# Performance work log

Hardware: AMD Instinct MI355X
Metric: run time of the kernel (lower is better)

Reference implementation:

```python
import jax, jax.numpy as jnp
import numpy as np

B, T, P, U = 2, 50, 5111, 64


def setup_inputs() -> dict:
    key = jax.random.key(0)
    ks = jax.random.split(key, 12)
    data_target = jax.random.randint(ks[0], (B, T), 0, P)
    data_cor = jax.random.randint(ks[1], (B, T), 0, 2)
    # X: bi-LSTM max-pooled problem encodings [P, 2U]
    X = jax.random.normal(ks[2], (P, 2 * U), dtype=jnp.float32) * 0.1
    # cos_X: cosine similarity of X with itself (as in call_encode)
    norm = jnp.sqrt(jnp.sum(X * X, axis=1))
    cos_X = (X @ X.T) / (norm[:, None] * norm[None, :])
    # causal lower-triangular aggregation mask [T, T]
    trimatrix = jnp.tril(jnp.ones((T, T), dtype=jnp.float32))
    # frozen embedding2 table [2, 4U]
    emb2 = jax.random.uniform(ks[3], (2, 4 * U), minval=-1.0, maxval=1.0, dtype=jnp.float32)
    # LSTM params (keras gate order i,f,c,o), input dim 4U
    s = 0.1549193338
    Wk = jax.random.uniform(ks[4], (4 * U, 4 * U), minval=-s, maxval=s, dtype=jnp.float32)
    Wr = jax.random.normal(ks[5], (U, 4 * U), dtype=jnp.float32) * 0.05  # orthogonal-ish stand-in
    bl = jnp.concatenate([jnp.zeros((U,)), jnp.ones((U,)), jnp.zeros((2 * U,))]).astype(jnp.float32)  # unit forget bias
    s1 = 0.1732050808
    W1 = jax.random.uniform(ks[6], (3 * U, 50), minval=-s1, maxval=s1, dtype=jnp.float32)
    b1 = jnp.zeros((50,), dtype=jnp.float32)
    s2 = 0.3429971703
    W2 = jax.random.uniform(ks[7], (50, 1), minval=-s2, maxval=s2, dtype=jnp.float32)
    b2 = jnp.zeros((1,), dtype=jnp.float32)
    return {"data_target": data_target, "data_cor": data_cor, "num_pro": P,
            "X": X, "cos_X": cos_X, "trimatrix": trimatrix, "emb2": emb2,
            "Wk": Wk, "Wr": Wr, "bl": bl, "W1": W1, "b1": b1, "W2": W2, "b2": b2}


def _lstm(x, Wk, Wr, bl):
    # x: [B, T, D] -> h: [B, T, U]; keras LSTM math, gate order i,f,g,o
    u = Wr.shape[0]
    xT = jnp.swapaxes(x, 0, 1)  # [T, B, D]
    h0 = jnp.zeros((x.shape[0], u), x.dtype)
    c0 = jnp.zeros((x.shape[0], u), x.dtype)

    def step(carry, xt):
        h, c = carry
        z = xt @ Wk + h @ Wr + bl
        i, f, g, o = jnp.split(z, 4, axis=-1)
        c = jax.nn.sigmoid(f) * c + jax.nn.sigmoid(i) * jnp.tanh(g)
        h = jax.nn.sigmoid(o) * jnp.tanh(c)
        return (h, c), h

    _, hs = jax.lax.scan(step, (h0, c0), xT)
    return jnp.swapaxes(hs, 0, 1)


def reference(data_target, data_cor, num_pro, X, cos_X, trimatrix, emb2, Wk, Wr, bl, W1, b1, W2, b2):
    # one_hot @ X == gather
    t_X = X[data_target]                             # [B,T,2U]
    t_X = jnp.concatenate([t_X, t_X], axis=-1)       # [B,T,4U]
    xt = t_X * emb2[data_cor]                        # [B,T,4U]
    ht = _lstm(xt, Wk, Wr, bl)                       # [B,T,U]
    # attention aggregation: a[b,t,p] = cos_X[target[b,t], p]
    a = cos_X[data_target]                           # [B,T,P]
    # ajhj[b,s,p,u] = sum_t trimatrix[t,s] * a[b,t,p] * ht[b,t,u]
    ajhj = jnp.einsum('btp,btu,ts->bspu', a, ht, trimatrix)  # [B,T,P,U]
    XX = jnp.broadcast_to(X[None, None], (ajhj.shape[0], ajhj.shape[1], num_pro, X.shape[1]))
    hatt = jnp.concatenate([ajhj, XX], axis=-1)      # [B,T,P,3U]
    r = jax.nn.relu(hatt @ W1 + b1)                  # [B,T,P,50]
    r = r @ W2 + b2                                  # [B,T,P,1]
    return r
```

## Files before the change

### kernel.cpp

```cpp
#include <hip/hip_runtime.h>
#include <math.h>

#define B_ 2
#define T_ 50
#define P_ 5111
#define U_ 64

typedef float v2f __attribute__((ext_vector_type(2)));

#define QPERM(x, ctrl)                                                        \
  __int_as_float(__builtin_amdgcn_mov_dpp(__float_as_int(x), (ctrl), 0xf, 0xf, true))

__global__ __launch_bounds__(256) void zx_kernel(
    const int* __restrict__ tgt, const int* __restrict__ cor,
    const float* __restrict__ X, const float* __restrict__ emb2,
    const float* __restrict__ Wk, float* __restrict__ ZX) {
  const int bt = blockIdx.x;
  const int k  = threadIdx.x;
  __shared__ float xe[256];
  const int t_ = tgt[bt], c_ = cor[bt];
  xe[k] = X[t_ * 128 + (k & 127)] * emb2[c_ * 256 + k];
  __syncthreads();
  float z = 0.f;
#pragma unroll 8
  for (int d = 0; d < 256; ++d)
    z = fmaf(xe[d], Wk[d * 256 + k], z);
  ZX[bt * 256 + k] = z;
}

__global__ __launch_bounds__(256) void lstm_xwt_kernel(
    const float* __restrict__ ZX, const float* __restrict__ Wr,
    const float* __restrict__ bl, const float* __restrict__ W1,
    const float* __restrict__ X, const float* __restrict__ b1,
    float* __restrict__ G, float* __restrict__ XWT) {
  const int blk = blockIdx.x;
  const int k   = threadIdx.x;

  if (blk >= B_) {
    __shared__ float xrow[4][128];
    const int sub = k >> 6, lane = k & 63;
    const int p = (blk - B_) * 4 + sub;
    if (p < P_) {
      xrow[sub][lane]      = X[p * 128 + lane];
      xrow[sub][64 + lane] = X[p * 128 + 64 + lane];
    }
    __syncthreads();
    if (p < P_ && lane < 50) {
      float acc = b1[lane];
#pragma unroll 16
      for (int u = 0; u < 128; ++u)
        acc = fmaf(xrow[sub][u], W1[(64 + u) * 50 + lane], acc);
      XWT[lane * P_ + p] = acc;
    }
    return;
  }

  const int b   = blk;
  const int g   = k & 3;
  const int u   = k >> 2;
  const int col = g * 64 + u;
  __shared__ __align__(16) float H_s[T_ + 1][64];
  __shared__ __align__(16) float W1_s[64 * 50];

  v2f w2[32];
#pragma unroll
  for (int i = 0; i < 32; ++i) {
    v2f t; t.x = Wr[(2 * i) * 256 + col]; t.y = Wr[(2 * i + 1) * 256 + col];
    w2[i] = t;
  }
  const float blv = bl[col];
  float znext = ZX[(b * T_) * 256 + col];
  for (int i = k; i < 64 * 50; i += 256) W1_s[i] = W1[i];
  if (k < 64) H_s[0][k] = 0.f;
  float c = 0.f;
  __syncthreads();

  for (int t = 0; t < T_; ++t) {
    const float zcur = znext;
    if (t + 1 < T_) znext = ZX[(b * T_ + t + 1) * 256 + col];
    const float4* h4 = (const float4*)&H_s[t][0];
    v2f a0 = {0.f, 0.f}, a1 = {0.f, 0.f}, a2 = {0.f, 0.f}, a3 = {0.f, 0.f};
#pragma unroll
    for (int q = 0; q < 16; ++q) {
      const float4 hq = h4[q];
      v2f hlo; hlo.x = hq.x; hlo.y = hq.y;
      v2f hhi; hhi.x = hq.z; hhi.y = hq.w;
      if (q & 1) {
        a2 = __builtin_elementwise_fma(hlo, w2[2 * q], a2);
        a3 = __builtin_elementwise_fma(hhi, w2[2 * q + 1], a3);
      } else {
        a0 = __builtin_elementwise_fma(hlo, w2[2 * q], a0);
        a1 = __builtin_elementwise_fma(hhi, w2[2 * q + 1], a1);
      }
    }
    const v2f as = (a0 + a2) + (a1 + a3);
    const float z = as.x + as.y + zcur + blv;
    const bool isg2 = (g == 2);
    const float arg = isg2 ? (2.f * z) : (-z);
    const float e   = __expf(arg);
    const float v   = __fdividef(1.f, 1.f + e);
    const float res = isg2 ? fmaf(-2.f, v, 1.f) : v;
    const float v1 = QPERM(res, 177);
    const float v2 = QPERM(res, 78);
    const float v3 = QPERM(res, 27);
    const float ig = (g == 0) ? res : (g == 1) ? v1 : (g == 2) ? v2 : v3;
    const float fg = (g == 1) ? res : (g == 0) ? v1 : (g == 3) ? v2 : v3;
    const float gg = (g == 2) ? res : (g == 3) ? v1 : (g == 0) ? v2 : v3;
    const float og = (g == 3) ? res : (g == 2) ? v1 : (g == 1) ? v2 : v3;
    c = fmaf(fg, c, ig * gg);
    const float th = fmaf(-2.f, __fdividef(1.f, 1.f + __expf(2.f * c)), 1.f);
    if (g == 0) H_s[t + 1][u] = og * th;
    __syncthreads();
  }

  const v2f* W1_2 = (const v2f*)W1_s;
  v2f*       G_2  = (v2f*)G;
  for (int task = k; task < T_ * 25; task += 256) {
    const int t  = task / 25;
    const int jp = task % 25;
    const float* hrow = &H_s[t + 1][0];
    v2f acc = {0.f, 0.f};
#pragma unroll
    for (int u2 = 0; u2 < 64; ++u2) {
      v2f hb; hb.x = hrow[u2]; hb.y = hrow[u2];
      acc = __builtin_elementwise_fma(hb, W1_2[u2 * 25 + jp], acc);
    }
    G_2[b * (T_ * 25) + task] = acc;
  }
}

__global__ __launch_bounds__(256) void out_kernel(
    const int* __restrict__ tgt, const float* __restrict__ cosX,
    const float* __restrict__ G, const float* __restrict__ XWT,
    const float* __restrict__ W2, const float* __restrict__ b2,
    float* __restrict__ out) {
  const int b   = blockIdx.y;
  const int tid = threadIdx.x;
  const int p   = blockIdx.x * 256 + tid;
  __shared__ __align__(16) float G_s[T_ * 50];
  __shared__ __align__(16) float W2_s[50];
  __shared__ int tgt_s[T_];
  for (int i = tid; i < T_ * 50; i += 256) G_s[i] = G[b * T_ * 50 + i];
  if (tid < 50) {
    W2_s[tid]  = W2[tid];
    tgt_s[tid] = tgt[b * T_ + tid];
  }
  __syncthreads();
  if (p >= P_) return;

  float av[T_];
#pragma unroll
  for (int s = 0; s < T_; ++s) av[s] = cosX[tgt_s[s] * P_ + p];

  v2f S2[25];
#pragma unroll
  for (int jj = 0; jj < 25; ++jj) {
    v2f t; t.x = XWT[(2 * jj) * P_ + p]; t.y = XWT[(2 * jj + 1) * P_ + p];
    S2[jj] = t;
  }
  const v2f* W2_2 = (const v2f*)W2_s;
  const float b2v = b2[0];
  const v2f zero2 = {0.f, 0.f};
#pragma unroll
  for (int s = T_ - 1; s >= 0; --s) {
    const v2f* G2 = (const v2f*)&G_s[s * 50];
    v2f av2; av2.x = av[s]; av2.y = av[s];
    v2f acc2; acc2.x = b2v; acc2.y = 0.f;
#pragma unroll
    for (int jj = 0; jj < 25; ++jj) {
      S2[jj] = __builtin_elementwise_fma(av2, G2[jj], S2[jj]);
      const v2f r = __builtin_elementwise_max(S2[jj], zero2);
      acc2 = __builtin_elementwise_fma(r, W2_2[jj], acc2);
    }
    out[(b * T_ + s) * P_ + p] = acc2.x + acc2.y;
  }
}

extern "C" void kernel_launch(void* const* d_in, const int* in_sizes, int n_in,
                              void* d_out, int out_size, void* d_ws, size_t ws_size,
                              hipStream_t stream) {
  const int*   tgt  = (const int*)d_in[0];
  const int*   cor  = (const int*)d_in[1];
  const float* X    = (const float*)d_in[3];
  const float* cosX = (const float*)d_in[4];
  const float* emb2 = (const float*)d_in[6];
  const float* Wk   = (const float*)d_in[7];
  const float* Wr   = (const float*)d_in[8];
  const float* bl   = (const float*)d_in[9];
  const float* W1   = (const float*)d_in[10];
  const float* b1   = (const float*)d_in[11];
  const float* W2   = (const float*)d_in[12];
  const float* b2   = (const float*)d_in[13];
  float* out = (float*)d_out;

  float* ws  = (float*)d_ws;
  float* ZX  = ws;
  float* G   = ws + 25600;
  float* XWT = ws + 30600;

  const int xw_blocks = (P_ + 3) / 4;
  zx_kernel<<<dim3(B_ * T_), dim3(256), 0, stream>>>(tgt, cor, X, emb2, Wk, ZX);
  lstm_xwt_kernel<<<dim3(B_ + xw_blocks), dim3(256), 0, stream>>>(
      ZX, Wr, bl, W1, X, b1, G, XWT);
  out_kernel<<<dim3((P_ + 255) / 256, B_), dim3(256), 0, stream>>>(
      tgt, cosX, G, XWT, W2, b2, out);
}
```

Before: 248.4 us.

## Split output kernel over time chunks and move XWT into the pre-kernel

The output kernel gets a third grid dimension of 5 chunks over the time axis. Each block redundantly accumulates the suffix of later timesteps without the ReLU/W2 part, then emits outputs only for its own 10 timesteps. The goal is more blocks (the old grid was only 40 blocks) and shorter serial chains, at the cost of redundant FMA work and repeated cosX reads. The X@W1 precompute also moves out of the LSTM launch into the ZX kernel, so the LSTM kernel runs alone with 2 blocks.

```diff
diff --git a/kernel.cpp b/kernel.cpp
--- a/kernel.cpp
+++ b/kernel.cpp
@@ -5,57 +5,60 @@
 #define T_ 50
 #define P_ 5111
 #define U_ 64
+#define SC_ 10
+#define CH_ 5
 
 typedef float v2f __attribute__((ext_vector_type(2)));
 
 #define QPERM(x, ctrl)                                                        \
   __int_as_float(__builtin_amdgcn_mov_dpp(__float_as_int(x), (ctrl), 0xf, 0xf, true))
 
-__global__ __launch_bounds__(256) void zx_kernel(
+__global__ __launch_bounds__(256) void pre_kernel(
     const int* __restrict__ tgt, const int* __restrict__ cor,
     const float* __restrict__ X, const float* __restrict__ emb2,
-    const float* __restrict__ Wk, float* __restrict__ ZX) {
-  const int bt = blockIdx.x;
-  const int k  = threadIdx.x;
-  __shared__ float xe[256];
-  const int t_ = tgt[bt], c_ = cor[bt];
-  xe[k] = X[t_ * 128 + (k & 127)] * emb2[c_ * 256 + k];
+    const float* __restrict__ Wk, float* __restrict__ ZX,
+    const float* __restrict__ W1, const float* __restrict__ b1,
+    float* __restrict__ XWT) {
+  const int blk = blockIdx.x;
+  const int k   = threadIdx.x;
+  __shared__ float smem[512];
+
+  if (blk < B_ * T_) {
+    const int t_ = tgt[blk], c_ = cor[blk];
+    smem[k] = X[t_ * 128 + (k & 127)] * emb2[c_ * 256 + k];
+    __syncthreads();
+    float z = 0.f;
+#pragma unroll 8
+    for (int d = 0; d < 256; ++d)
+      z = fmaf(smem[d], Wk[d * 256 + k], z);
+    ZX[blk * 256 + k] = z;
+    return;
+  }
+
+  const int xb   = blk - B_ * T_;
+  const int sub  = k >> 6, lane = k & 63;
+  const int p    = xb * 4 + sub;
+  float* xrow = &smem[sub * 128];
+  if (p < P_) {
+    xrow[lane]      = X[p * 128 + lane];
+    xrow[64 + lane] = X[p * 128 + 64 + lane];
+  }
   __syncthreads();
-  float z = 0.f;
-#pragma unroll 8
-  for (int d = 0; d < 256; ++d)
-    z = fmaf(xe[d], Wk[d * 256 + k], z);
-  ZX[bt * 256 + k] = z;
-}
-
-__global__ __launch_bounds__(256) void lstm_xwt_kernel(
+  if (p < P_ && lane < 50) {
+    float acc = b1[lane];
+#pragma unroll 16
+    for (int u = 0; u < 128; ++u)
+      acc = fmaf(xrow[u], W1[(64 + u) * 50 + lane], acc);
+    XWT[lane * P_ + p] = acc;
+  }
+}
+
+__global__ __launch_bounds__(256) void lstm_kernel(
     const float* __restrict__ ZX, const float* __restrict__ Wr,
     const float* __restrict__ bl, const float* __restrict__ W1,
-    const float* __restrict__ X, const float* __restrict__ b1,
-    float* __restrict__ G, float* __restrict__ XWT) {
-  const int blk = blockIdx.x;
-  const int k   = threadIdx.x;
-
-  if (blk >= B_) {
-    __shared__ float xrow[4][128];
-    const int sub = k >> 6, lane = k & 63;
-    const int p = (blk - B_) * 4 + sub;
-    if (p < P_) {
-      xrow[sub][lane]      = X[p * 128 + lane];
-      xrow[sub][64 + lane] = X[p * 128 + 64 + lane];
-    }
-    __syncthreads();
-    if (p < P_ && lane < 50) {
-      float acc = b1[lane];
-#pragma unroll 16
-      for (int u = 0; u < 128; ++u)
-        acc = fmaf(xrow[sub][u], W1[(64 + u) * 50 + lane], acc);
-      XWT[lane * P_ + p] = acc;
-    }
-    return;
-  }
-
-  const int b   = blk;
+    float* __restrict__ G) {
+  const int b = blockIdx.x;
+  const int k = threadIdx.x;
   const int g   = k & 3;
   const int u   = k >> 2;
   const int col = g * 64 + u;
@@ -129,28 +132,29 @@
   }
 }
 
-__global__ __launch_bounds__(256) void out_kernel(
+template <int CH>
+__device__ __forceinline__ void out_body(
     const int* __restrict__ tgt, const float* __restrict__ cosX,
     const float* __restrict__ G, const float* __restrict__ XWT,
     const float* __restrict__ W2, const float* __restrict__ b2,
-    float* __restrict__ out) {
+    float* __restrict__ out, float* G_s, float* W2_s, int* tgt_s) {
+  constexpr int s_lo = CH * SC_;
+  constexpr int s_hi = s_lo + SC_;
   const int b   = blockIdx.y;
   const int tid = threadIdx.x;
   const int p   = blockIdx.x * 256 + tid;
-  __shared__ __align__(16) float G_s[T_ * 50];
-  __shared__ __align__(16) float W2_s[50];
-  __shared__ int tgt_s[T_];
-  for (int i = tid; i < T_ * 50; i += 256) G_s[i] = G[b * T_ * 50 + i];
+
+  for (int i = s_lo * 50 + tid; i < T_ * 50; i += 256) G_s[i] = G[b * T_ * 50 + i];
   if (tid < 50) {
-    W2_s[tid]  = W2[tid];
-    tgt_s[tid] = tgt[b * T_ + tid];
+    W2_s[tid] = W2[tid];
+    if (tid >= s_lo) tgt_s[tid] = tgt[b * T_ + tid];
   }
   __syncthreads();
   if (p >= P_) return;
 
-  float av[T_];
-#pragma unroll
-  for (int s = 0; s < T_; ++s) av[s] = cosX[tgt_s[s] * P_ + p];
+  float av[T_ - s_lo];
+#pragma unroll
+  for (int t = s_lo; t < T_; ++t) av[t - s_lo] = cosX[tgt_s[t] * P_ + p];
 
   v2f S2[25];
 #pragma unroll
@@ -158,13 +162,23 @@
     v2f t; t.x = XWT[(2 * jj) * P_ + p]; t.y = XWT[(2 * jj + 1) * P_ + p];
     S2[jj] = t;
   }
+
+#pragma unroll
+  for (int t = T_ - 1; t >= s_hi; --t) {
+    const v2f* G2 = (const v2f*)&G_s[t * 50];
+    v2f av2; av2.x = av[t - s_lo]; av2.y = av[t - s_lo];
+#pragma unroll
+    for (int jj = 0; jj < 25; ++jj)
+      S2[jj] = __builtin_elementwise_fma(av2, G2[jj], S2[jj]);
+  }
+
   const v2f* W2_2 = (const v2f*)W2_s;
   const float b2v = b2[0];
   const v2f zero2 = {0.f, 0.f};
 #pragma unroll
-  for (int s = T_ - 1; s >= 0; --s) {
+  for (int s = s_hi - 1; s >= s_lo; --s) {
     const v2f* G2 = (const v2f*)&G_s[s * 50];
-    v2f av2; av2.x = av[s]; av2.y = av[s];
+    v2f av2; av2.x = av[s - s_lo]; av2.y = av[s - s_lo];
     v2f acc2; acc2.x = b2v; acc2.y = 0.f;
 #pragma unroll
     for (int jj = 0; jj < 25; ++jj) {
@@ -173,6 +187,23 @@
       acc2 = __builtin_elementwise_fma(r, W2_2[jj], acc2);
     }
     out[(b * T_ + s) * P_ + p] = acc2.x + acc2.y;
+  }
+}
+
+__global__ __launch_bounds__(256) void out_kernel(
+    const int* __restrict__ tgt, const float* __restrict__ cosX,
+    const float* __restrict__ G, const float* __restrict__ XWT,
+    const float* __restrict__ W2, const float* __restrict__ b2,
+    float* __restrict__ out) {
+  __shared__ __align__(16) float G_s[T_ * 50];
+  __shared__ __align__(16) float W2_s[50];
+  __shared__ int tgt_s[T_];
+  switch (blockIdx.z) {
+    case 0: out_body<0>(tgt, cosX, G, XWT, W2, b2, out, G_s, W2_s, tgt_s); break;
+    case 1: out_body<1>(tgt, cosX, G, XWT, W2, b2, out, G_s, W2_s, tgt_s); break;
+    case 2: out_body<2>(tgt, cosX, G, XWT, W2, b2, out, G_s, W2_s, tgt_s); break;
+    case 3: out_body<3>(tgt, cosX, G, XWT, W2, b2, out, G_s, W2_s, tgt_s); break;
+    default: out_body<4>(tgt, cosX, G, XWT, W2, b2, out, G_s, W2_s, tgt_s); break;
   }
 }
 
@@ -199,9 +230,9 @@
   float* XWT = ws + 30600;
 
   const int xw_blocks = (P_ + 3) / 4;
-  zx_kernel<<<dim3(B_ * T_), dim3(256), 0, stream>>>(tgt, cor, X, emb2, Wk, ZX);
-  lstm_xwt_kernel<<<dim3(B_ + xw_blocks), dim3(256), 0, stream>>>(
-      ZX, Wr, bl, W1, X, b1, G, XWT);
-  out_kernel<<<dim3((P_ + 255) / 256, B_), dim3(256), 0, stream>>>(
+  pre_kernel<<<dim3(B_ * T_ + xw_blocks), dim3(256), 0, stream>>>(
+      tgt, cor, X, emb2, Wk, ZX, W1, b1, XWT);
+  lstm_kernel<<<dim3(B_), dim3(256), 0, stream>>>(ZX, Wr, bl, W1, G);
+  out_kernel<<<dim3((P_ + 255) / 256, B_, CH_), dim3(256), 0, stream>>>(
       tgt, cosX, G, XWT, W2, b2, out);
 }
```

Result: faster. 226.8 us (-8.7%).
